# Performance work log

Hardware: AMD Instinct MI355X
Metric: run time of the kernel (lower is better)

Reference implementation:

```python
import jax, jax.numpy as jnp
import numpy as np

B, C, Q, H = 64, 1024, 128, 256


def setup_inputs() -> dict:
    key = jax.random.key(0)
    k1, k2, k3 = jax.random.split(key, 3)
    return {
        "context": jax.random.normal(k1, (B, C, H), dtype=jnp.float32),
        "context_mask": jnp.ones((B, C), dtype=jnp.int32),
        "query": jax.random.normal(k2, (B, Q, H), dtype=jnp.float32),
        "query_mask": jnp.ones((B, Q), dtype=jnp.int32),
        "att_w": jax.random.normal(k3, (3 * H,), dtype=jnp.float32) / np.sqrt(3.0 * H).astype(np.float32),
        "att_b": jnp.zeros((), dtype=jnp.float32),
    }


def reference(context, context_mask, query, query_mask, att_w, att_b):
    # Dropout is identity in eval mode. Masks are declared but unused in the
    # original forward; kept in the signature for parity.
    h = context.shape[-1]
    w_c, w_q, w_m = att_w[:h], att_w[h:2 * h], att_w[2 * h:]
    # sim_matrix: Linear on concat([c, q, c*q]) decomposes into three projections
    # -> never materialize the (B,C,Q,3H) tensor.
    sim = (context @ w_c)[:, :, None] \
        + (query @ w_q)[:, None, :] \
        + jnp.einsum('bch,bqh->bcq', context * w_m, query) \
        + att_b  # (B, C, Q)
    # context-to-query attention
    alpha = jax.nn.softmax(sim, axis=-1)                 # (B, C, Q)
    a = jnp.einsum('bcq,bqh->bch', alpha, query)         # (B, C, H)
    # query-to-context attention
    beta = jax.nn.softmax(jnp.max(sim, axis=-1), axis=-1)  # (B, C)
    b = jnp.einsum('bc,bch->bh', beta, context)[:, None, :]  # (B, 1, H)
    b = jnp.broadcast_to(b, context.shape)               # (B, C, H)
    return jnp.concatenate([context, a, context * a, context * b], axis=-1)  # (B, C, 8H)
```

## Files before the change

### kernel.cpp

```cpp
#include <hip/hip_runtime.h>

#define B_ 64
#define C_ 1024
#define Q_ 128
#define H_ 256

typedef __attribute__((ext_vector_type(8))) short bfrag;
typedef __attribute__((ext_vector_type(4))) float f32x4;

__device__ __forceinline__ short f2bf(float f) {
    union { float f; unsigned u; } v; v.f = f;
    unsigned u = v.u;
    unsigned r = u + 0x7fffu + ((u >> 16) & 1u);
    return (short)(r >> 16);
}
__device__ __forceinline__ float bf2f(short s) {
    union { float f; unsigned u; } v;
    v.u = ((unsigned)(unsigned short)s) << 16;
    return v.f;
}

__global__ __launch_bounds__(256) void k_qdot(
    const float* __restrict__ qry, const float* __restrict__ attw,
    const float* __restrict__ attb, float* __restrict__ qdot)
{
    const int tid = threadIdx.x, lane = tid & 63, w = tid >> 6;
    const int bid = blockIdx.x;
    const int b = bid >> 5, qg = bid & 31;
    const int q = qg * 4 + w;
    const float* src = qry + ((size_t)b * Q_ + q) * H_ + lane * 4;
    f32x4 v = *(const f32x4*)src;
    f32x4 wv = *(const f32x4*)(attw + H_ + lane * 4);
    float p = v.x * wv.x + v.y * wv.y + v.z * wv.z + v.w * wv.w;
    #pragma unroll
    for (int d = 1; d < 64; d <<= 1) p += __shfl_xor(p, d);
    if (lane == 0) qdot[b * Q_ + q] = p + attb[0];
}

#define SPAD 40
#define PPAD 136

__global__ __launch_bounds__(256) void k_sim(
    const float* __restrict__ ctx,
    const float* __restrict__ qry,
    const float* __restrict__ attw,
    const float* __restrict__ qdot,
    float* __restrict__ smax,
    float* __restrict__ out)
{
    __shared__ float wm_s[H_];
    __shared__ float wc_s[H_];
    __shared__ float qd_s[Q_];
    __shared__ float cdot_s[64];
    __shared__ short qh_s[Q_][SPAD];
    __shared__ short ql_s[Q_][SPAD];
    __shared__ short ch_s[64][SPAD];
    __shared__ short cl_s[64][SPAD];
    __shared__ short P_s[64][PPAD];

    const int tid = threadIdx.x;
    const int lane = tid & 63;
    const int w = tid >> 6;
    const int bid = blockIdx.x;
    const int b = bid >> 4;
    const int c0 = (bid & 15) * 64;

    wc_s[tid] = attw[tid];
    wm_s[tid] = attw[2 * H_ + tid];
    if (tid < Q_) qd_s[tid] = qdot[b * Q_ + tid];
    __syncthreads();

    const int r16 = lane & 15;
    const int kp  = lane >> 4;

    f32x4 acc[8];
    #pragma unroll
    for (int t = 0; t < 8; ++t) acc[t] = (f32x4)(0.f);

    float cdp = 0.f;

    const int crow = tid >> 2;
    const int ckof = (tid & 3) * 8;
    const int qrow = tid >> 1;
    const int qkof = (tid & 1) * 16;

    const float* ctxb = ctx + ((size_t)b * C_ + c0) * H_;
    const float* qryb = qry + (size_t)b * Q_ * H_;

    for (int k0 = 0; k0 < H_; k0 += 32) {
        {
            const float* src = ctxb + crow * H_ + k0 + ckof;
            f32x4 v0 = *(const f32x4*)(src);
            f32x4 v1 = *(const f32x4*)(src + 4);
            float tv[8];
            *(f32x4*)&tv[0] = v0;
            *(f32x4*)&tv[4] = v1;
            bfrag hv, lv;
            #pragma unroll
            for (int j = 0; j < 8; ++j) {
                int k = k0 + ckof + j;
                cdp += tv[j] * wc_s[k];
                float cm = tv[j] * wm_s[k];
                short hi = f2bf(cm);
                hv[j] = hi;
                lv[j] = f2bf(cm - bf2f(hi));
            }
            *(bfrag*)&ch_s[crow][ckof] = hv;
            *(bfrag*)&cl_s[crow][ckof] = lv;
        }
        {
            const float* src = qryb + qrow * H_ + k0 + qkof;
            f32x4 v0 = *(const f32x4*)(src);
            f32x4 v1 = *(const f32x4*)(src + 4);
            f32x4 v2 = *(const f32x4*)(src + 8);
            f32x4 v3 = *(const f32x4*)(src + 12);
            float tv[16];
            *(f32x4*)&tv[0]  = v0;
            *(f32x4*)&tv[4]  = v1;
            *(f32x4*)&tv[8]  = v2;
            *(f32x4*)&tv[12] = v3;
            bfrag h0v, l0v, h1v, l1v;
            #pragma unroll
            for (int j = 0; j < 8; ++j) {
                short hi = f2bf(tv[j]);
                h0v[j] = hi;
                l0v[j] = f2bf(tv[j] - bf2f(hi));
            }
            #pragma unroll
            for (int j = 0; j < 8; ++j) {
                short hi = f2bf(tv[8 + j]);
                h1v[j] = hi;
                l1v[j] = f2bf(tv[8 + j] - bf2f(hi));
            }
            *(bfrag*)&qh_s[qrow][qkof]     = h0v;
            *(bfrag*)&ql_s[qrow][qkof]     = l0v;
            *(bfrag*)&qh_s[qrow][qkof + 8] = h1v;
            *(bfrag*)&ql_s[qrow][qkof + 8] = l1v;
        }
        __syncthreads();
        bfrag a_hi = *(bfrag*)&ch_s[w * 16 + r16][kp * 8];
        bfrag a_lo = *(bfrag*)&cl_s[w * 16 + r16][kp * 8];
        #pragma unroll
        for (int t = 0; t < 8; ++t) {
            bfrag b_hi = *(bfrag*)&qh_s[t * 16 + r16][kp * 8];
            bfrag b_lo = *(bfrag*)&ql_s[t * 16 + r16][kp * 8];
            acc[t] = __builtin_amdgcn_mfma_f32_16x16x32_bf16(a_hi, b_hi, acc[t], 0, 0, 0);
            acc[t] = __builtin_amdgcn_mfma_f32_16x16x32_bf16(a_lo, b_hi, acc[t], 0, 0, 0);
            acc[t] = __builtin_amdgcn_mfma_f32_16x16x32_bf16(a_hi, b_lo, acc[t], 0, 0, 0);
        }
        __syncthreads();
    }

    {
        float cv = cdp;
        cv += __shfl_xor(cv, 1);
        cv += __shfl_xor(cv, 2);
        if ((lane & 3) == 0) cdot_s[crow] = cv;
    }
    __syncthreads();

    float qdv[8];
    #pragma unroll
    for (int t = 0; t < 8; ++t) qdv[t] = qd_s[t * 16 + r16];
    float cdv[4];
    #pragma unroll
    for (int r = 0; r < 4; ++r) cdv[r] = cdot_s[w * 16 + kp * 4 + r];

    #pragma unroll
    for (int r = 0; r < 4; ++r) {
        float ev[8];
        float m = -1e30f;
        #pragma unroll
        for (int t = 0; t < 8; ++t) {
            float s = acc[t][r] + cdv[r] + qdv[t];
            ev[t] = s;
            m = fmaxf(m, s);
        }
        m = fmaxf(m, __shfl_xor(m, 1));
        m = fmaxf(m, __shfl_xor(m, 2));
        m = fmaxf(m, __shfl_xor(m, 4));
        m = fmaxf(m, __shfl_xor(m, 8));
        float ssum = 0.f;
        #pragma unroll
        for (int t = 0; t < 8; ++t) {
            float e = __expf(ev[t] - m);
            ev[t] = e;
            ssum += e;
        }
        ssum += __shfl_xor(ssum, 1);
        ssum += __shfl_xor(ssum, 2);
        ssum += __shfl_xor(ssum, 4);
        ssum += __shfl_xor(ssum, 8);
        const int rr = w * 16 + kp * 4 + r;
        if (r16 == 0) smax[(size_t)b * C_ + c0 + rr] = m;
        float inv = 1.f / ssum;
        #pragma unroll
        for (int t = 0; t < 8; ++t)
            P_s[rr][t * 16 + r16] = f2bf(ev[t] * inv);
    }
    __syncthreads();

    f32x4 a2[4][4];
    #pragma unroll
    for (int m = 0; m < 4; ++m)
        #pragma unroll
        for (int i = 0; i < 4; ++i) a2[m][i] = (f32x4)(0.f);

    const int h0w = w * 64;
    for (int kq = 0; kq < 4; ++kq) {
        bfrag ap[4];
        #pragma unroll
        for (int m = 0; m < 4; ++m)
            ap[m] = *(bfrag*)&P_s[m * 16 + r16][kq * 32 + kp * 8];
        #pragma unroll
        for (int i = 0; i < 4; ++i) {
            const float* qc = qryb + (size_t)(kq * 32 + kp * 8) * H_ + h0w + i * 16 + r16;
            bfrag bq;
            #pragma unroll
            for (int j = 0; j < 8; ++j) bq[j] = f2bf(qc[(size_t)j * H_]);
            #pragma unroll
            for (int m = 0; m < 4; ++m)
                a2[m][i] = __builtin_amdgcn_mfma_f32_16x16x32_bf16(ap[m], bq, a2[m][i], 0, 0, 0);
        }
    }

    #pragma unroll
    for (int m = 0; m < 4; ++m) {
        #pragma unroll
        for (int r = 0; r < 4; ++r) {
            const int cl = m * 16 + kp * 4 + r;
            const size_t orow = ((size_t)b * C_ + c0 + cl) * (4 * H_);
            const float* crow_p = ctxb + (size_t)cl * H_;
            #pragma unroll
            for (int i = 0; i < 4; ++i) {
                const int h = h0w + i * 16 + r16;
                float av = a2[m][i][r];
                float cvx = crow_p[h];
                out[orow + h] = cvx;
                out[orow + H_ + h] = av;
                out[orow + 2 * H_ + h] = cvx * av;
            }
        }
    }
}

__global__ __launch_bounds__(256) void k_beta(
    const float* __restrict__ ctx, const float* __restrict__ smax,
    float* __restrict__ bpart)
{
    __shared__ float beta_s[C_];
    __shared__ float red_s[8];
    const int tid = threadIdx.x, lane = tid & 63, w = tid >> 6;
    const int bid = blockIdx.x;
    const int b = bid >> 2, quad = bid & 3;

    f32x4 v = *(const f32x4*)(smax + (size_t)b * C_ + tid * 4);
    float m = fmaxf(fmaxf(v.x, v.y), fmaxf(v.z, v.w));
    #pragma unroll
    for (int d = 1; d < 64; d <<= 1) m = fmaxf(m, __shfl_xor(m, d));
    if (lane == 0) red_s[w] = m;
    __syncthreads();
    m = fmaxf(fmaxf(red_s[0], red_s[1]), fmaxf(red_s[2], red_s[3]));

    f32x4 e;
    e.x = __expf(v.x - m); e.y = __expf(v.y - m);
    e.z = __expf(v.z - m); e.w = __expf(v.w - m);
    float s = e.x + e.y + e.z + e.w;
    #pragma unroll
    for (int d = 1; d < 64; d <<= 1) s += __shfl_xor(s, d);
    if (lane == 0) red_s[4 + w] = s;
    __syncthreads();
    s = red_s[4] + red_s[5] + red_s[6] + red_s[7];
    float inv = 1.f / s;
    *(f32x4*)&beta_s[tid * 4] = e * inv;
    __syncthreads();

    const float* cb = ctx + ((size_t)b * C_ + quad * 256) * H_ + tid;
    float acc = 0.f;
    #pragma unroll 8
    for (int i = 0; i < 256; ++i)
        acc += beta_s[quad * 256 + i] * cb[(size_t)i * H_];
    bpart[(size_t)bid * H_ + tid] = acc;
}

__global__ __launch_bounds__(256) void k_colb(
    const float* __restrict__ ctx, const float* __restrict__ bpart,
    float* __restrict__ out)
{
    const int tid = threadIdx.x;
    const int bid = blockIdx.x;
    const int b = bid >> 8, cg = bid & 255;
    const int c = cg * 4 + (tid >> 6);
    const int h = (tid & 63) * 4;

    const float* bp = bpart + (size_t)b * 4 * H_ + h;
    f32x4 bv = *(const f32x4*)bp;
    bv += *(const f32x4*)(bp + H_);
    bv += *(const f32x4*)(bp + 2 * H_);
    bv += *(const f32x4*)(bp + 3 * H_);

    const size_t rowi = (size_t)b * C_ + c;
    f32x4 cv = *(const f32x4*)(ctx + rowi * H_ + h);
    *(f32x4*)(out + rowi * (4 * H_) + 3 * H_ + h) = cv * bv;
}

extern "C" void kernel_launch(void* const* d_in, const int* in_sizes, int n_in,
                              void* d_out, int out_size, void* d_ws, size_t ws_size,
                              hipStream_t stream) {
    const float* ctx  = (const float*)d_in[0];
    const float* qry  = (const float*)d_in[2];
    const float* attw = (const float*)d_in[4];
    const float* attb = (const float*)d_in[5];
    float* out = (float*)d_out;

    float* qdot  = (float*)d_ws;
    float* smax  = qdot + B_ * Q_;
    float* bpart = smax + B_ * C_;

    k_qdot<<<B_ * 32, 256, 0, stream>>>(qry, attw, attb, qdot);
    k_sim<<<B_ * 16, 256, 0, stream>>>(ctx, qry, attw, qdot, smax, out);
    k_beta<<<B_ * 4, 256, 0, stream>>>(ctx, smax, bpart);
    k_colb<<<B_ * 256, 256, 0, stream>>>(ctx, bpart, out);
}
```

Baseline: 383.8 us.

## Precompute bf16 hi/lo and transposed query once per batch in prep kernel

A new prep kernel converts query to bf16 hi/lo split arrays and a transposed bf16 copy in workspace, and also folds in the query-dot computation. The sim kernel then loads these precomputed fragments directly instead of converting fp32 query in every one of its 16 blocks per batch, and reads the PV operand with vector loads from the transposed copy instead of strided scalar fp32 loads. The output write is restaged through shared memory so stores become coalesced float4 rows. This costs extra workspace traffic and a fallback path when the workspace is too small.

```diff
diff --git a/kernel.cpp b/kernel.cpp
--- a/kernel.cpp
+++ b/kernel.cpp
@@ -18,6 +18,74 @@
     union { float f; unsigned u; } v;
     v.u = ((unsigned)(unsigned short)s) << 16;
     return v.f;
+}
+
+__global__ __launch_bounds__(256) void k_prep(
+    const float* __restrict__ qry, const float* __restrict__ attw,
+    const float* __restrict__ attb,
+    short* __restrict__ qh, short* __restrict__ ql, short* __restrict__ qT,
+    float* __restrict__ qdot)
+{
+    __shared__ float wq_s[H_];
+    __shared__ short t_s[64][80];
+    const int tid = threadIdx.x;
+    const int bid = blockIdx.x;
+    const int b = bid >> 1;
+    const int q0 = (bid & 1) * 64;
+    wq_s[tid] = attw[H_ + tid];
+    __syncthreads();
+
+    const int rloc = tid >> 2;
+    const int row = q0 + rloc;
+    const int colseg = (tid & 3) * 16;
+    const float* src_base = qry + ((size_t)b * Q_ + row) * H_;
+    float qp = 0.f;
+
+    for (int ct = 0; ct < 4; ++ct) {
+        const int c0 = ct * 64;
+        float tv[16];
+        *(f32x4*)&tv[0]  = *(const f32x4*)(src_base + c0 + colseg);
+        *(f32x4*)&tv[4]  = *(const f32x4*)(src_base + c0 + colseg + 4);
+        *(f32x4*)&tv[8]  = *(const f32x4*)(src_base + c0 + colseg + 8);
+        *(f32x4*)&tv[12] = *(const f32x4*)(src_base + c0 + colseg + 12);
+        bfrag hv0, lv0, hv1, lv1;
+        #pragma unroll
+        for (int j = 0; j < 8; ++j) {
+            qp += tv[j] * wq_s[c0 + colseg + j];
+            short hi = f2bf(tv[j]);
+            hv0[j] = hi; lv0[j] = f2bf(tv[j] - bf2f(hi));
+        }
+        #pragma unroll
+        for (int j = 0; j < 8; ++j) {
+            float t = tv[8 + j];
+            qp += t * wq_s[c0 + colseg + 8 + j];
+            short hi = f2bf(t);
+            hv1[j] = hi; lv1[j] = f2bf(t - bf2f(hi));
+        }
+        short* qh_p = qh + ((size_t)b * Q_ + row) * H_ + c0 + colseg;
+        *(bfrag*)qh_p = hv0; *(bfrag*)(qh_p + 8) = hv1;
+        short* ql_p = ql + ((size_t)b * Q_ + row) * H_ + c0 + colseg;
+        *(bfrag*)ql_p = lv0; *(bfrag*)(ql_p + 8) = lv1;
+        #pragma unroll
+        for (int j = 0; j < 8; ++j) {
+            t_s[colseg + j][rloc] = hv0[j];
+            t_s[colseg + 8 + j][rloc] = hv1[j];
+        }
+        __syncthreads();
+        {
+            const int hl = tid >> 2;
+            const int qs = (tid & 3) * 16;
+            bfrag tv2 = *(bfrag*)&t_s[hl][qs];
+            bfrag tv3 = *(bfrag*)&t_s[hl][qs + 8];
+            short* dst = &qT[((size_t)b * H_ + c0 + hl) * Q_ + q0 + qs];
+            *(bfrag*)dst = tv2;
+            *(bfrag*)(dst + 8) = tv3;
+        }
+        __syncthreads();
+    }
+    qp += __shfl_xor(qp, 1);
+    qp += __shfl_xor(qp, 2);
+    if ((tid & 3) == 0) qdot[b * Q_ + row] = qp + attb[0];
 }
 
 __global__ __launch_bounds__(256) void k_qdot(
@@ -39,14 +107,210 @@
 
 #define SPAD 40
 #define PPAD 136
+#define APAD 268
 
 __global__ __launch_bounds__(256) void k_sim(
     const float* __restrict__ ctx,
-    const float* __restrict__ qry,
+    const short* __restrict__ qh_g,
+    const short* __restrict__ ql_g,
+    const short* __restrict__ qT,
     const float* __restrict__ attw,
     const float* __restrict__ qdot,
     float* __restrict__ smax,
     float* __restrict__ out)
+{
+    __shared__ union SM {
+        struct {
+            short qh[Q_][SPAD];
+            short ql[Q_][SPAD];
+            short ch[64][SPAD];
+            short cl[64][SPAD];
+        } st;
+        float a_s[16][APAD];
+    } u;
+    __shared__ short P_s[64][PPAD];
+    __shared__ float wm_s[H_];
+    __shared__ float wc_s[H_];
+    __shared__ float qd_s[Q_];
+    __shared__ float cdot_s[64];
+
+    const int tid = threadIdx.x;
+    const int lane = tid & 63;
+    const int w = tid >> 6;
+    const int bid = blockIdx.x;
+    const int b = bid >> 4;
+    const int c0 = (bid & 15) * 64;
+
+    wc_s[tid] = attw[tid];
+    wm_s[tid] = attw[2 * H_ + tid];
+    if (tid < Q_) qd_s[tid] = qdot[b * Q_ + tid];
+    __syncthreads();
+
+    const int r16 = lane & 15;
+    const int kp  = lane >> 4;
+
+    f32x4 acc[8];
+    #pragma unroll
+    for (int t = 0; t < 8; ++t) acc[t] = (f32x4)(0.f);
+
+    float cdp = 0.f;
+
+    const int crow = tid >> 2;
+    const int ckof = (tid & 3) * 8;
+    const int qrow = tid >> 1;
+    const int qkof = (tid & 1) * 16;
+
+    const float* ctxb = ctx + ((size_t)b * C_ + c0) * H_;
+    const short* qhb = qh_g + (size_t)b * Q_ * H_;
+    const short* qlb = ql_g + (size_t)b * Q_ * H_;
+
+    for (int k0 = 0; k0 < H_; k0 += 32) {
+        {
+            const float* src = ctxb + crow * H_ + k0 + ckof;
+            f32x4 v0 = *(const f32x4*)(src);
+            f32x4 v1 = *(const f32x4*)(src + 4);
+            float tv[8];
+            *(f32x4*)&tv[0] = v0;
+            *(f32x4*)&tv[4] = v1;
+            bfrag hv, lv;
+            #pragma unroll
+            for (int j = 0; j < 8; ++j) {
+                int k = k0 + ckof + j;
+                cdp += tv[j] * wc_s[k];
+                float cm = tv[j] * wm_s[k];
+                short hi = f2bf(cm);
+                hv[j] = hi;
+                lv[j] = f2bf(cm - bf2f(hi));
+            }
+            *(bfrag*)&u.st.ch[crow][ckof] = hv;
+            *(bfrag*)&u.st.cl[crow][ckof] = lv;
+        }
+        {
+            const short* qhp = &qhb[qrow * H_ + k0 + qkof];
+            const short* qlp = &qlb[qrow * H_ + k0 + qkof];
+            *(bfrag*)&u.st.qh[qrow][qkof]     = *(const bfrag*)qhp;
+            *(bfrag*)&u.st.qh[qrow][qkof + 8] = *(const bfrag*)(qhp + 8);
+            *(bfrag*)&u.st.ql[qrow][qkof]     = *(const bfrag*)qlp;
+            *(bfrag*)&u.st.ql[qrow][qkof + 8] = *(const bfrag*)(qlp + 8);
+        }
+        __syncthreads();
+        bfrag a_hi = *(bfrag*)&u.st.ch[w * 16 + r16][kp * 8];
+        bfrag a_lo = *(bfrag*)&u.st.cl[w * 16 + r16][kp * 8];
+        #pragma unroll
+        for (int t = 0; t < 8; ++t) {
+            bfrag b_hi = *(bfrag*)&u.st.qh[t * 16 + r16][kp * 8];
+            bfrag b_lo = *(bfrag*)&u.st.ql[t * 16 + r16][kp * 8];
+            acc[t] = __builtin_amdgcn_mfma_f32_16x16x32_bf16(a_hi, b_hi, acc[t], 0, 0, 0);
+            acc[t] = __builtin_amdgcn_mfma_f32_16x16x32_bf16(a_lo, b_hi, acc[t], 0, 0, 0);
+            acc[t] = __builtin_amdgcn_mfma_f32_16x16x32_bf16(a_hi, b_lo, acc[t], 0, 0, 0);
+        }
+        __syncthreads();
+    }
+
+    {
+        float cv = cdp;
+        cv += __shfl_xor(cv, 1);
+        cv += __shfl_xor(cv, 2);
+        if ((lane & 3) == 0) cdot_s[crow] = cv;
+    }
+    __syncthreads();
+
+    float qdv[8];
+    #pragma unroll
+    for (int t = 0; t < 8; ++t) qdv[t] = qd_s[t * 16 + r16];
+    float cdv[4];
+    #pragma unroll
+    for (int r = 0; r < 4; ++r) cdv[r] = cdot_s[w * 16 + kp * 4 + r];
+
+    #pragma unroll
+    for (int r = 0; r < 4; ++r) {
+        float ev[8];
+        float m = -1e30f;
+        #pragma unroll
+        for (int t = 0; t < 8; ++t) {
+            float s = acc[t][r] + cdv[r] + qdv[t];
+            ev[t] = s;
+            m = fmaxf(m, s);
+        }
+        m = fmaxf(m, __shfl_xor(m, 1));
+        m = fmaxf(m, __shfl_xor(m, 2));
+        m = fmaxf(m, __shfl_xor(m, 4));
+        m = fmaxf(m, __shfl_xor(m, 8));
+        float ssum = 0.f;
+        #pragma unroll
+        for (int t = 0; t < 8; ++t) {
+            float e = __expf(ev[t] - m);
+            ev[t] = e;
+            ssum += e;
+        }
+        ssum += __shfl_xor(ssum, 1);
+        ssum += __shfl_xor(ssum, 2);
+        ssum += __shfl_xor(ssum, 4);
+        ssum += __shfl_xor(ssum, 8);
+        const int rr = w * 16 + kp * 4 + r;
+        if (r16 == 0) smax[(size_t)b * C_ + c0 + rr] = m;
+        float inv = 1.f / ssum;
+        #pragma unroll
+        for (int t = 0; t < 8; ++t)
+            P_s[rr][t * 16 + r16] = f2bf(ev[t] * inv);
+    }
+    __syncthreads();
+
+    f32x4 a2[4][4];
+    #pragma unroll
+    for (int m = 0; m < 4; ++m)
+        #pragma unroll
+        for (int i = 0; i < 4; ++i) a2[m][i] = (f32x4)(0.f);
+
+    const int h0w = w * 64;
+    const short* qTb = qT + (size_t)b * H_ * Q_;
+    #pragma unroll
+    for (int kq = 0; kq < 4; ++kq) {
+        bfrag ap[4];
+        #pragma unroll
+        for (int m = 0; m < 4; ++m)
+            ap[m] = *(bfrag*)&P_s[m * 16 + r16][kq * 32 + kp * 8];
+        #pragma unroll
+        for (int i = 0; i < 4; ++i) {
+            bfrag bq = *(const bfrag*)&qTb[(size_t)(h0w + i * 16 + r16) * Q_ + kq * 32 + kp * 8];
+            #pragma unroll
+            for (int m = 0; m < 4; ++m)
+                a2[m][i] = __builtin_amdgcn_mfma_f32_16x16x32_bf16(ap[m], bq, a2[m][i], 0, 0, 0);
+        }
+    }
+
+    #pragma unroll
+    for (int m = 0; m < 4; ++m) {
+        #pragma unroll
+        for (int i = 0; i < 4; ++i)
+            #pragma unroll
+            for (int r = 0; r < 4; ++r)
+                u.a_s[kp * 4 + r][w * 64 + i * 16 + r16] = a2[m][i][r];
+        __syncthreads();
+        {
+            const int row = tid >> 4;
+            const int seg = tid & 15;
+            const int cl = m * 16 + row;
+            const size_t orow = ((size_t)b * C_ + c0 + cl) * (4 * H_);
+            const float* cp = ctxb + (size_t)cl * H_ + seg * 16;
+            float* op = out + orow + seg * 16;
+            #pragma unroll
+            for (int k2 = 0; k2 < 4; ++k2) {
+                f32x4 cvx = *(const f32x4*)(cp + k2 * 4);
+                f32x4 av = *(const f32x4*)&u.a_s[row][seg * 16 + k2 * 4];
+                *(f32x4*)(op + k2 * 4) = cvx;
+                *(f32x4*)(op + H_ + k2 * 4) = av;
+                *(f32x4*)(op + 2 * H_ + k2 * 4) = cvx * av;
+            }
+        }
+        __syncthreads();
+    }
+}
+
+__global__ __launch_bounds__(256) void k_sim_v1(
+    const float* __restrict__ ctx, const float* __restrict__ qry,
+    const float* __restrict__ attw, const float* __restrict__ qdot,
+    float* __restrict__ smax, float* __restrict__ out)
 {
     __shared__ float wm_s[H_];
     __shared__ float wc_s[H_];
@@ -76,14 +340,9 @@
     f32x4 acc[8];
     #pragma unroll
     for (int t = 0; t < 8; ++t) acc[t] = (f32x4)(0.f);
-
     float cdp = 0.f;
-
-    const int crow = tid >> 2;
-    const int ckof = (tid & 3) * 8;
-    const int qrow = tid >> 1;
-    const int qkof = (tid & 1) * 16;
-
+    const int crow = tid >> 2, ckof = (tid & 3) * 8;
+    const int qrow = tid >> 1, qkof = (tid & 1) * 16;
     const float* ctxb = ctx + ((size_t)b * C_ + c0) * H_;
     const float* qryb = qry + (size_t)b * Q_ * H_;
 
@@ -93,8 +352,7 @@
             f32x4 v0 = *(const f32x4*)(src);
             f32x4 v1 = *(const f32x4*)(src + 4);
             float tv[8];
-            *(f32x4*)&tv[0] = v0;
-            *(f32x4*)&tv[4] = v1;
+            *(f32x4*)&tv[0] = v0; *(f32x4*)&tv[4] = v1;
             bfrag hv, lv;
             #pragma unroll
             for (int j = 0; j < 8; ++j) {
@@ -102,35 +360,28 @@
                 cdp += tv[j] * wc_s[k];
                 float cm = tv[j] * wm_s[k];
                 short hi = f2bf(cm);
-                hv[j] = hi;
-                lv[j] = f2bf(cm - bf2f(hi));
+                hv[j] = hi; lv[j] = f2bf(cm - bf2f(hi));
             }
             *(bfrag*)&ch_s[crow][ckof] = hv;
             *(bfrag*)&cl_s[crow][ckof] = lv;
         }
         {
             const float* src = qryb + qrow * H_ + k0 + qkof;
-            f32x4 v0 = *(const f32x4*)(src);
-            f32x4 v1 = *(const f32x4*)(src + 4);
-            f32x4 v2 = *(const f32x4*)(src + 8);
-            f32x4 v3 = *(const f32x4*)(src + 12);
             float tv[16];
-            *(f32x4*)&tv[0]  = v0;
-            *(f32x4*)&tv[4]  = v1;
-            *(f32x4*)&tv[8]  = v2;
-            *(f32x4*)&tv[12] = v3;
+            *(f32x4*)&tv[0]  = *(const f32x4*)(src);
+            *(f32x4*)&tv[4]  = *(const f32x4*)(src + 4);
+            *(f32x4*)&tv[8]  = *(const f32x4*)(src + 8);
+            *(f32x4*)&tv[12] = *(const f32x4*)(src + 12);
             bfrag h0v, l0v, h1v, l1v;
             #pragma unroll
             for (int j = 0; j < 8; ++j) {
                 short hi = f2bf(tv[j]);
-                h0v[j] = hi;
-                l0v[j] = f2bf(tv[j] - bf2f(hi));
+                h0v[j] = hi; l0v[j] = f2bf(tv[j] - bf2f(hi));
             }
             #pragma unroll
             for (int j = 0; j < 8; ++j) {
                 short hi = f2bf(tv[8 + j]);
-                h1v[j] = hi;
-                l1v[j] = f2bf(tv[8 + j] - bf2f(hi));
+                h1v[j] = hi; l1v[j] = f2bf(tv[8 + j] - bf2f(hi));
             }
             *(bfrag*)&qh_s[qrow][qkof]     = h0v;
             *(bfrag*)&ql_s[qrow][qkof]     = l0v;
@@ -150,7 +401,6 @@
         }
         __syncthreads();
     }
-
     {
         float cv = cdp;
         cv += __shfl_xor(cv, 1);
@@ -158,14 +408,12 @@
         if ((lane & 3) == 0) cdot_s[crow] = cv;
     }
     __syncthreads();
-
     float qdv[8];
     #pragma unroll
     for (int t = 0; t < 8; ++t) qdv[t] = qd_s[t * 16 + r16];
     float cdv[4];
     #pragma unroll
     for (int r = 0; r < 4; ++r) cdv[r] = cdot_s[w * 16 + kp * 4 + r];
-
     #pragma unroll
     for (int r = 0; r < 4; ++r) {
         float ev[8];
@@ -173,8 +421,7 @@
         #pragma unroll
         for (int t = 0; t < 8; ++t) {
             float s = acc[t][r] + cdv[r] + qdv[t];
-            ev[t] = s;
-            m = fmaxf(m, s);
+            ev[t] = s; m = fmaxf(m, s);
         }
         m = fmaxf(m, __shfl_xor(m, 1));
         m = fmaxf(m, __shfl_xor(m, 2));
@@ -184,8 +431,7 @@
         #pragma unroll
         for (int t = 0; t < 8; ++t) {
             float e = __expf(ev[t] - m);
-            ev[t] = e;
-            ssum += e;
+            ev[t] = e; ssum += e;
         }
         ssum += __shfl_xor(ssum, 1);
         ssum += __shfl_xor(ssum, 2);
@@ -199,13 +445,11 @@
             P_s[rr][t * 16 + r16] = f2bf(ev[t] * inv);
     }
     __syncthreads();
-
     f32x4 a2[4][4];
     #pragma unroll
     for (int m = 0; m < 4; ++m)
         #pragma unroll
         for (int i = 0; i < 4; ++i) a2[m][i] = (f32x4)(0.f);
-
     const int h0w = w * 64;
     for (int kq = 0; kq < 4; ++kq) {
         bfrag ap[4];
@@ -223,7 +467,6 @@
                 a2[m][i] = __builtin_amdgcn_mfma_f32_16x16x32_bf16(ap[m], bq, a2[m][i], 0, 0, 0);
         }
     }
-
     #pragma unroll
     for (int m = 0; m < 4; ++m) {
         #pragma unroll
@@ -316,9 +559,20 @@
     float* qdot  = (float*)d_ws;
     float* smax  = qdot + B_ * Q_;
     float* bpart = smax + B_ * C_;
-
-    k_qdot<<<B_ * 32, 256, 0, stream>>>(qry, attw, attb, qdot);
-    k_sim<<<B_ * 16, 256, 0, stream>>>(ctx, qry, attw, qdot, smax, out);
+    short* qh    = (short*)(bpart + 256 * H_);
+    short* ql    = qh + (size_t)B_ * Q_ * H_;
+    short* qT    = ql + (size_t)B_ * Q_ * H_;
+
+    const size_t need = (size_t)(B_ * Q_ + B_ * C_ + 256 * H_) * 4
+                      + (size_t)3 * B_ * Q_ * H_ * 2;
+
+    if (ws_size >= need) {
+        k_prep<<<B_ * 2, 256, 0, stream>>>(qry, attw, attb, qh, ql, qT, qdot);
+        k_sim<<<B_ * 16, 256, 0, stream>>>(ctx, qh, ql, qT, attw, qdot, smax, out);
+    } else {
+        k_qdot<<<B_ * 32, 256, 0, stream>>>(qry, attw, attb, qdot);
+        k_sim_v1<<<B_ * 16, 256, 0, stream>>>(ctx, qry, attw, qdot, smax, out);
+    }
     k_beta<<<B_ * 4, 256, 0, stream>>>(ctx, smax, bpart);
     k_colb<<<B_ * 256, 256, 0, stream>>>(ctx, bpart, out);
 }
```

New measurement: 425.1 us. 1.11x slower.
